# Optimization experiments

Hardware: AMD Instinct MI355X
Metric: run time of the kernel (lower is better)

## Reference

```python
import math
import jax, jax.numpy as jnp
import numpy as np

N_HEADS = 16

def setup_inputs() -> dict:
    key = jax.random.key(0)
    k1, k2, k3 = jax.random.split(key, 3)
    B, T, C = 4, 2048, 1024
    alpha = 0.5
    std = alpha * (1.0 / C) ** 0.5
    x = jax.random.normal(k1, (B, T, C), dtype=jnp.float32)
    w_attn = jax.random.normal(k2, (C, 3 * C), dtype=jnp.float32) * std
    b_attn = jnp.zeros((3 * C,), dtype=jnp.float32)
    w_proj = jax.random.normal(k3, (C, C), dtype=jnp.float32) * std
    b_proj = jnp.zeros((C,), dtype=jnp.float32)
    return {"x": x, "w_attn": w_attn, "b_attn": b_attn, "w_proj": w_proj, "b_proj": b_proj}

def reference(x, w_attn, b_attn, w_proj, b_proj):
    B, T, C = x.shape
    H = N_HEADS
    D = C // H
    qkv = x @ w_attn + b_attn                      # [B,T,3C]
    q, k, v = jnp.split(qkv, 3, axis=-1)
    # [B,T,C] -> [B,H,T,D]
    q = q.reshape(B, T, H, D).transpose(0, 2, 1, 3)
    k = k.reshape(B, T, H, D).transpose(0, 2, 1, 3)
    v = v.reshape(B, T, H, D).transpose(0, 2, 1, 3)
    att = jnp.einsum('bhqd,bhkd->bhqk', q, k) * (1.0 / math.sqrt(D))
    causal = jnp.tril(jnp.ones((T, T), dtype=bool))
    att = jnp.where(causal, att, -jnp.inf)
    att = jax.nn.softmax(att, axis=-1)
    y = jnp.einsum('bhqk,bhkd->bhqd', att, v)      # [B,H,T,D]
    y = y.transpose(0, 2, 1, 3).reshape(B, T, C)
    return y @ w_proj + b_proj
```

## Files before the change

### kernel.cpp

```cpp
#include <hip/hip_runtime.h>
#include <hip/hip_bf16.h>

typedef __bf16 bf16x8 __attribute__((ext_vector_type(8)));
typedef float f32x4 __attribute__((ext_vector_type(4)));
typedef float f32x16 __attribute__((ext_vector_type(16)));
typedef unsigned short u16x8 __attribute__((ext_vector_type(8)));
typedef unsigned short u16x4 __attribute__((ext_vector_type(4)));

#define HB 16
#define TT 2048
#define CCH 1024
#define DD 64

#define AS1 __attribute__((address_space(1)))
#define AS3 __attribute__((address_space(3)))
#define GL16(gp, lp) __builtin_amdgcn_global_load_lds((const AS1 void*)(gp), (AS3 void*)(lp), 16, 0, 0)

__device__ __forceinline__ unsigned short f2bf(float f) {
  union { __hip_bfloat16 h; unsigned short u; } cv;
  cv.h = __float2bfloat16(f);
  return cv.u;
}

__device__ __forceinline__ unsigned pack2(float lo, float hi) {
  unsigned r;
  asm("v_cvt_pk_bf16_f32 %0, %1, %2" : "=v"(r) : "v"(lo), "v"(hi));
  return r;
}

__device__ __forceinline__ f32x4 mfma16(bf16x8 a, bf16x8 b, f32x4 c) {
  return __builtin_amdgcn_mfma_f32_16x16x32_bf16(a, b, c, 0, 0, 0);
}
__device__ __forceinline__ f32x16 mfma32(bf16x8 a, bf16x8 b, f32x16 c) {
  return __builtin_amdgcn_mfma_f32_32x32x16_bf16(a, b, c, 0, 0, 0);
}

__device__ __forceinline__ f32x16 zero16() {
  f32x16 z;
  #pragma unroll
  for (int r = 0; r < 16; ++r) z[r] = 0.f;
  return z;
}


__global__ __launch_bounds__(256) void cvt_f32_bf16(const float* __restrict__ in,
                                                    unsigned short* __restrict__ out,
                                                    int n4) {
  int i = blockIdx.x * 256 + threadIdx.x;
  if (i >= n4) return;
  float4 v = reinterpret_cast<const float4*>(in)[i];
  u16x4 o;
  o.x = f2bf(v.x); o.y = f2bf(v.y); o.z = f2bf(v.z); o.w = f2bf(v.w);
  *reinterpret_cast<u16x4*>(out + (size_t)i * 4) = o;
}

__global__ __launch_bounds__(256) void transpose_cvt(const float* __restrict__ w,
                                                     unsigned short* __restrict__ wt,
                                                     int N) {
  __shared__ unsigned short t[32][33];
  int nb = blockIdx.x * 32, kb = blockIdx.y * 32;
  int tx = threadIdx.x & 31, ty = threadIdx.x >> 5;
  #pragma unroll
  for (int r = 0; r < 32; r += 8)
    t[ty + r][tx] = f2bf(w[(size_t)(kb + ty + r) * N + nb + tx]);
  __syncthreads();
  #pragma unroll
  for (int r = 0; r < 32; r += 8)
    wt[(size_t)(nb + ty + r) * 1024 + kb + tx] = t[tx][ty + r];
}


template <int EPI>
__global__ __launch_bounds__(256) void gemm_bf16(
    const unsigned short* __restrict__ A,
    const unsigned short* __restrict__ Bt,
    const float* __restrict__ bias,
    float* __restrict__ outf,
    unsigned short* __restrict__ qb,
    unsigned short* __restrict__ kb,
    unsigned short* __restrict__ vt,
    int nbx, int wpx) {
  __shared__ unsigned short As[8192];
  __shared__ unsigned short Bs[8192];
  const int bid = blockIdx.x;
  const int work = (bid & 7) * wpx + (bid >> 3);
  const int m0 = (work / nbx) * 128, n0 = (work % nbx) * 128;
  const int tid = threadIdx.x;
  const int lane = tid & 63;
  const int wid = tid >> 6;
  const int r16 = lane & 15, g = lane >> 4;
  const int wm = wid >> 1, wn = wid & 1;
  const int srow = tid >> 3;
  const int schx = (tid & 7) ^ (srow & 7);

  f32x4 acc[4][4];
  #pragma unroll
  for (int i = 0; i < 4; ++i)
    #pragma unroll
    for (int j = 0; j < 4; ++j) acc[i][j] = (f32x4){0.f, 0.f, 0.f, 0.f};

  const int rx = r16 & 7;

  for (int kt = 0; kt < 1024; kt += 64) {
    #pragma unroll
    for (int i = 0; i < 4; ++i) {
      const int row = i * 32 + srow;
      GL16(A + (size_t)(m0 + row) * 1024 + kt + schx * 8, As + i * 2048 + tid * 8);
    }
    #pragma unroll
    for (int i = 0; i < 4; ++i) {
      const int row = i * 32 + srow;
      GL16(Bt + (size_t)(n0 + row) * 1024 + kt + schx * 8, Bs + i * 2048 + tid * 8);
    }
    __syncthreads();
    #pragma unroll
    for (int h = 0; h < 2; ++h) {
      bf16x8 af[4], bfr[4];
      #pragma unroll
      for (int i = 0; i < 4; ++i)
        af[i] = *reinterpret_cast<const bf16x8*>(
            &As[(wm * 64 + i * 16 + r16) * 64 + ((g + 4 * h) ^ rx) * 8]);
      #pragma unroll
      for (int j = 0; j < 4; ++j)
        bfr[j] = *reinterpret_cast<const bf16x8*>(
            &Bs[(wn * 64 + j * 16 + r16) * 64 + ((g + 4 * h) ^ rx) * 8]);
      #pragma unroll
      for (int i = 0; i < 4; ++i)
        #pragma unroll
        for (int j = 0; j < 4; ++j)
          acc[i][j] = mfma16(af[i], bfr[j], acc[i][j]);
    }
    __syncthreads();
  }

  #pragma unroll
  for (int i = 0; i < 4; ++i) {
    #pragma unroll
    for (int j = 0; j < 4; ++j) {
      const int n = n0 + wn * 64 + j * 16 + r16;
      const int mbase = m0 + wm * 64 + i * 16 + g * 4;
      const float bi = bias[n];
      if (EPI == 1) {
        #pragma unroll
        for (int r = 0; r < 4; ++r)
          outf[(size_t)(mbase + r) * 1024 + n] = acc[i][j][r] + bi;
      } else {
        const int which = n >> 10;
        const int cc2 = n & 1023;
        const int h = cc2 >> 6, d = cc2 & 63;
        const int b = mbase >> 11, t = mbase & 2047;
        if (which == 2) {
          u16x4 o;
          #pragma unroll
          for (int r = 0; r < 4; ++r) o[r] = f2bf(acc[i][j][r] + bi);
          *reinterpret_cast<u16x4*>(
              &vt[(((size_t)b * HB + h) * DD + d) * TT + t]) = o;
        } else {
          unsigned short* dst = (which == 0) ? qb : kb;
          const float sc = (which == 0) ? 0.18033688011112042f : 1.0f;
          #pragma unroll
          for (int r = 0; r < 4; ++r)
            dst[(((size_t)b * HB + h) * TT + (t + r)) * DD + d] =
                f2bf((acc[i][j][r] + bi) * sc);
        }
      }
    }
  }
}


__global__ __launch_bounds__(256, 2) void attn_kernel(
    const unsigned short* __restrict__ qg_,
    const unsigned short* __restrict__ kg_,
    const unsigned short* __restrict__ vtg_,
    unsigned short* __restrict__ yb) {
  const int bid = blockIdx.x;
  const int work = (bid & 7) * 64 + (bid >> 3);
  const int bh = work >> 3;
  const int jb = work & 7;
  const int tid = threadIdx.x;
  const int wid = tid >> 6;
  const int lane = tid & 63;
  const int l31 = lane & 31, h = lane >> 5;
  const int lx = lane & 7;
  const unsigned short* Q = qg_ + (size_t)bh * TT * DD;
  const unsigned short* K = kg_ + (size_t)bh * TT * DD;
  const unsigned short* Vt = vtg_ + (size_t)bh * DD * TT;
  const int b = bh >> 4, hd = bh & 15;

  __shared__ unsigned short kbuf[2][4096];
  __shared__ unsigned short vbuf[2][4096];

  const int krow0 = tid >> 3;
  const int chx = (tid & 7) ^ (krow0 & 7);

#define SK(bi_, kvb_) do {                                                   \
    const unsigned short* gk_ = K + (size_t)((kvb_) + krow0) * DD + chx * 8; \
    GL16(gk_,            &kbuf[bi_][tid * 8]);                               \
    GL16(gk_ + 32 * DD,  &kbuf[bi_][2048 + tid * 8]);                        \
  } while (0)
#define SV(bi_, kvb_) do {                                                   \
    const unsigned short* gv_ = Vt + (size_t)krow0 * TT + (kvb_) + chx * 8;  \
    GL16(gv_,            &vbuf[bi_][tid * 8]);                               \
    GL16(gv_ + 32 * TT,  &vbuf[bi_][2048 + tid * 8]);                        \
  } while (0)

  #pragma unroll
  for (int part = 0; part < 2; ++part) {
    const int qg0 = (part == 0) ? jb * 128 : (15 - jb) * 128;
    const int nt = (part == 0) ? (jb + 1) * 2 : (16 - jb) * 2;
    const int qw = qg0 + wid * 32;
    const int q = qw + l31;
    const int ntw = ((qw + 31) >> 6) + 1;

    bf16x8 qf[4];
    #pragma unroll
    for (int c = 0; c < 4; ++c)
      qf[c] = *reinterpret_cast<const bf16x8*>(&Q[(size_t)q * DD + c * 16 + h * 8]);

    f32x16 y0 = zero16(), y1 = zero16();
    float lp = 0.f;

    __syncthreads();
    SK(0, 0);
    SV(0, 0);
    if (nt > 1) {
      SK(1, 64);
      SV(1, 64);
      asm volatile("s_waitcnt vmcnt(4)" ::: "memory");
    } else {
      asm volatile("s_waitcnt vmcnt(0)" ::: "memory");
    }
    __builtin_amdgcn_s_barrier();

    for (int t = 0; t < nt; ++t) {
      const unsigned short* sK = kbuf[t & 1];
      const unsigned short* sV = vbuf[t & 1];

      if (t < ntw) {
        const int kvb = t * 64;

        f32x16 z0 = zero16(), z1 = zero16();
        __builtin_amdgcn_s_setprio(1);
        #pragma unroll
        for (int c = 0; c < 4; ++c) {
          bf16x8 kf = *reinterpret_cast<const bf16x8*>(
              &sK[l31 * 64 + (((2 * c + h) ^ lx)) * 8]);
          z0 = mfma32(kf, qf[c], z0);
        }
        #pragma unroll
        for (int c = 0; c < 4; ++c) {
          bf16x8 kf = *reinterpret_cast<const bf16x8*>(
              &sK[(32 + l31) * 64 + (((2 * c + h) ^ lx)) * 8]);
          z1 = mfma32(kf, qf[c], z1);
        }
        __builtin_amdgcn_s_setprio(0);

        if (t == ntw - 1) {
          #pragma unroll
          for (int r = 0; r < 16; ++r) {
            const int kv0 = kvb + (r & 3) + 8 * (r >> 2) + 4 * h;
            if (kv0 > q) z0[r] = -1e30f;
            if (kv0 + 32 > q) z1[r] = -1e30f;
          }
        }

        float sq[8];
        #pragma unroll
        for (int i = 0; i < 4; ++i) {
          #pragma unroll
          for (int r = 0; r < 4; ++r) {
            z0[4 * i + r] = exp2f(z0[4 * i + r]);
            z1[4 * i + r] = exp2f(z1[4 * i + r]);
          }
          sq[i] = (z0[4 * i] + z0[4 * i + 1]) + (z0[4 * i + 2] + z0[4 * i + 3]);
          sq[4 + i] = (z1[4 * i] + z1[4 * i + 1]) + (z1[4 * i + 2] + z1[4 * i + 3]);
        }
        lp += ((sq[0] + sq[1]) + (sq[2] + sq[3])) +
              ((sq[4] + sq[5]) + (sq[6] + sq[7]));

        unsigned pw[16];
        #pragma unroll
        for (int w = 0; w < 8; ++w) {
          pw[w] = pack2(z0[2 * w], z0[2 * w + 1]);
          pw[8 + w] = pack2(z1[2 * w], z1[2 * w + 1]);
        }
        #pragma unroll
        for (int kb = 0; kb < 4; ++kb) {
          asm("v_permlane32_swap_b32 %0, %1"
              : "+v"(pw[4 * kb]), "+v"(pw[4 * kb + 2]));
          asm("v_permlane32_swap_b32 %0, %1"
              : "+v"(pw[4 * kb + 1]), "+v"(pw[4 * kb + 3]));
        }

        __builtin_amdgcn_s_setprio(1);
        #pragma unroll
        for (int kb = 0; kb < 4; ++kb) {
          union { unsigned w[4]; bf16x8 v; } pf;
          pf.w[0] = pw[4 * kb];
          pf.w[1] = pw[4 * kb + 1];
          pf.w[2] = pw[4 * kb + 2];
          pf.w[3] = pw[4 * kb + 3];
          bf16x8 vf0 = *reinterpret_cast<const bf16x8*>(
              &sV[l31 * 64 + (((2 * kb + h) ^ lx)) * 8]);
          y0 = mfma32(vf0, pf.v, y0);
          bf16x8 vf1 = *reinterpret_cast<const bf16x8*>(
              &sV[(32 + l31) * 64 + (((2 * kb + h) ^ lx)) * 8]);
          y1 = mfma32(vf1, pf.v, y1);
        }
        __builtin_amdgcn_s_setprio(0);
      }

      __syncthreads();
      if (t + 2 < nt) {
        SK(t & 1, (t + 2) * 64);
        SV(t & 1, (t + 2) * 64);
      }
    }

    lp += __shfl_xor(lp, 32);
    const float rl = 1.0f / lp;
    const size_t obase = ((size_t)b * TT + q) * CCH + hd * DD;
    #pragma unroll
    for (int g4 = 0; g4 < 4; ++g4) {
      const int d0 = 8 * g4 + 4 * h;
      unsigned w0 = pack2(y0[4 * g4] * rl, y0[4 * g4 + 1] * rl);
      unsigned w1 = pack2(y0[4 * g4 + 2] * rl, y0[4 * g4 + 3] * rl);
      *reinterpret_cast<uint2*>(&yb[obase + d0]) = make_uint2(w0, w1);
      unsigned w2 = pack2(y1[4 * g4] * rl, y1[4 * g4 + 1] * rl);
      unsigned w3 = pack2(y1[4 * g4 + 2] * rl, y1[4 * g4 + 3] * rl);
      *reinterpret_cast<uint2*>(&yb[obase + 32 + d0]) = make_uint2(w2, w3);
    }
  }
#undef SK
#undef SV
}


extern "C" void kernel_launch(void* const* d_in, const int* in_sizes, int n_in,
                              void* d_out, int out_size, void* d_ws, size_t ws_size,
                              hipStream_t stream) {
  const float* x      = (const float*)d_in[0];
  const float* w_attn = (const float*)d_in[1];
  const float* b_attn = (const float*)d_in[2];
  const float* w_proj = (const float*)d_in[3];
  const float* b_proj = (const float*)d_in[4];
  float* out = (float*)d_out;
  char* ws = (char*)d_ws;

  unsigned short* xb  = (unsigned short*)(ws + 0);
  unsigned short* wat = (unsigned short*)(ws + 16777216);
  unsigned short* wpt = (unsigned short*)(ws + 23068672);
  unsigned short* qb  = (unsigned short*)(ws + 25165824);
  unsigned short* kb  = (unsigned short*)(ws + 41943040);
  unsigned short* vt  = (unsigned short*)(ws + 58720256);
  unsigned short* yb  = (unsigned short*)(ws + 75497472);

  cvt_f32_bf16<<<(8192 * 1024 / 4 + 255) / 256, 256, 0, stream>>>(x, xb, 8192 * 1024 / 4);
  transpose_cvt<<<dim3(3072 / 32, 32), 256, 0, stream>>>(w_attn, wat, 3072);
  transpose_cvt<<<dim3(1024 / 32, 32), 256, 0, stream>>>(w_proj, wpt, 1024);

  gemm_bf16<0><<<1536, 256, 0, stream>>>(
      xb, wat, b_attn, nullptr, qb, kb, vt, 24, 192);

  attn_kernel<<<512, 256, 0, stream>>>(qb, kb, vt, yb);

  gemm_bf16<1><<<512, 256, 0, stream>>>(
      yb, wpt, b_proj, out, nullptr, nullptr, nullptr, 8, 64);
}
```

Measured before the change: 175.8 us.

## Drop LDS K/V staging in attention; per-wave global loads with balanced strips

Rewrites the attention kernel so each wave loads K and V tiles directly from global memory instead of cooperatively staging them into double-buffered shared memory. Work is split into 32-row query strips assigned per wave with complementary causal lengths, and the grid doubles while occupancy hint rises to 4 blocks per CU. This removes barriers and LDS traffic but gives up cross-wave reuse of K/V, increasing global/cache load traffic and exposing load latency.

```diff
diff --git a/kernel.cpp b/kernel.cpp
--- a/kernel.cpp
+++ b/kernel.cpp
@@ -169,171 +169,120 @@
 }
 
 
-__global__ __launch_bounds__(256, 2) void attn_kernel(
+__global__ __launch_bounds__(256, 4) void attn_kernel(
     const unsigned short* __restrict__ qg_,
     const unsigned short* __restrict__ kg_,
     const unsigned short* __restrict__ vtg_,
     unsigned short* __restrict__ yb) {
   const int bid = blockIdx.x;
-  const int work = (bid & 7) * 64 + (bid >> 3);
-  const int bh = work >> 3;
-  const int jb = work & 7;
-  const int tid = threadIdx.x;
-  const int wid = tid >> 6;
-  const int lane = tid & 63;
+  const int work = (bid & 7) * 128 + (bid >> 3);
+  const int bh = work >> 4;
+  const int jb = work & 15;
+  const int wid = threadIdx.x >> 6;
+  const int lane = threadIdx.x & 63;
   const int l31 = lane & 31, h = lane >> 5;
-  const int lx = lane & 7;
-  const unsigned short* Q = qg_ + (size_t)bh * TT * DD;
-  const unsigned short* K = kg_ + (size_t)bh * TT * DD;
-  const unsigned short* Vt = vtg_ + (size_t)bh * DD * TT;
+  const int s = (wid == 0) ? jb : (wid == 1) ? (31 - jb)
+              : (wid == 2) ? (32 + jb) : (63 - jb);
+  const unsigned short* __restrict__ Q = qg_ + (size_t)bh * TT * DD;
+  const unsigned short* __restrict__ K = kg_ + (size_t)bh * TT * DD;
+  const unsigned short* __restrict__ Vt = vtg_ + (size_t)bh * DD * TT;
   const int b = bh >> 4, hd = bh & 15;
 
-  __shared__ unsigned short kbuf[2][4096];
-  __shared__ unsigned short vbuf[2][4096];
-
-  const int krow0 = tid >> 3;
-  const int chx = (tid & 7) ^ (krow0 & 7);
-
-#define SK(bi_, kvb_) do {                                                   \
-    const unsigned short* gk_ = K + (size_t)((kvb_) + krow0) * DD + chx * 8; \
-    GL16(gk_,            &kbuf[bi_][tid * 8]);                               \
-    GL16(gk_ + 32 * DD,  &kbuf[bi_][2048 + tid * 8]);                        \
-  } while (0)
-#define SV(bi_, kvb_) do {                                                   \
-    const unsigned short* gv_ = Vt + (size_t)krow0 * TT + (kvb_) + chx * 8;  \
-    GL16(gv_,            &vbuf[bi_][tid * 8]);                               \
-    GL16(gv_ + 32 * TT,  &vbuf[bi_][2048 + tid * 8]);                        \
-  } while (0)
-
-  #pragma unroll
-  for (int part = 0; part < 2; ++part) {
-    const int qg0 = (part == 0) ? jb * 128 : (15 - jb) * 128;
-    const int nt = (part == 0) ? (jb + 1) * 2 : (16 - jb) * 2;
-    const int qw = qg0 + wid * 32;
-    const int q = qw + l31;
-    const int ntw = ((qw + 31) >> 6) + 1;
-
-    bf16x8 qf[4];
-    #pragma unroll
-    for (int c = 0; c < 4; ++c)
-      qf[c] = *reinterpret_cast<const bf16x8*>(&Q[(size_t)q * DD + c * 16 + h * 8]);
-
-    f32x16 y0 = zero16(), y1 = zero16();
-    float lp = 0.f;
-
-    __syncthreads();
-    SK(0, 0);
-    SV(0, 0);
-    if (nt > 1) {
-      SK(1, 64);
-      SV(1, 64);
-      asm volatile("s_waitcnt vmcnt(4)" ::: "memory");
-    } else {
-      asm volatile("s_waitcnt vmcnt(0)" ::: "memory");
-    }
-    __builtin_amdgcn_s_barrier();
-
-    for (int t = 0; t < nt; ++t) {
-      const unsigned short* sK = kbuf[t & 1];
-      const unsigned short* sV = vbuf[t & 1];
-
-      if (t < ntw) {
-        const int kvb = t * 64;
-
-        f32x16 z0 = zero16(), z1 = zero16();
-        __builtin_amdgcn_s_setprio(1);
-        #pragma unroll
-        for (int c = 0; c < 4; ++c) {
-          bf16x8 kf = *reinterpret_cast<const bf16x8*>(
-              &sK[l31 * 64 + (((2 * c + h) ^ lx)) * 8]);
-          z0 = mfma32(kf, qf[c], z0);
-        }
-        #pragma unroll
-        for (int c = 0; c < 4; ++c) {
-          bf16x8 kf = *reinterpret_cast<const bf16x8*>(
-              &sK[(32 + l31) * 64 + (((2 * c + h) ^ lx)) * 8]);
-          z1 = mfma32(kf, qf[c], z1);
-        }
-        __builtin_amdgcn_s_setprio(0);
-
-        if (t == ntw - 1) {
-          #pragma unroll
-          for (int r = 0; r < 16; ++r) {
-            const int kv0 = kvb + (r & 3) + 8 * (r >> 2) + 4 * h;
-            if (kv0 > q) z0[r] = -1e30f;
-            if (kv0 + 32 > q) z1[r] = -1e30f;
-          }
-        }
-
-        float sq[8];
-        #pragma unroll
-        for (int i = 0; i < 4; ++i) {
-          #pragma unroll
-          for (int r = 0; r < 4; ++r) {
-            z0[4 * i + r] = exp2f(z0[4 * i + r]);
-            z1[4 * i + r] = exp2f(z1[4 * i + r]);
-          }
-          sq[i] = (z0[4 * i] + z0[4 * i + 1]) + (z0[4 * i + 2] + z0[4 * i + 3]);
-          sq[4 + i] = (z1[4 * i] + z1[4 * i + 1]) + (z1[4 * i + 2] + z1[4 * i + 3]);
-        }
-        lp += ((sq[0] + sq[1]) + (sq[2] + sq[3])) +
-              ((sq[4] + sq[5]) + (sq[6] + sq[7]));
-
-        unsigned pw[16];
-        #pragma unroll
-        for (int w = 0; w < 8; ++w) {
-          pw[w] = pack2(z0[2 * w], z0[2 * w + 1]);
-          pw[8 + w] = pack2(z1[2 * w], z1[2 * w + 1]);
-        }
-        #pragma unroll
-        for (int kb = 0; kb < 4; ++kb) {
-          asm("v_permlane32_swap_b32 %0, %1"
-              : "+v"(pw[4 * kb]), "+v"(pw[4 * kb + 2]));
-          asm("v_permlane32_swap_b32 %0, %1"
-              : "+v"(pw[4 * kb + 1]), "+v"(pw[4 * kb + 3]));
-        }
-
-        __builtin_amdgcn_s_setprio(1);
-        #pragma unroll
-        for (int kb = 0; kb < 4; ++kb) {
-          union { unsigned w[4]; bf16x8 v; } pf;
-          pf.w[0] = pw[4 * kb];
-          pf.w[1] = pw[4 * kb + 1];
-          pf.w[2] = pw[4 * kb + 2];
-          pf.w[3] = pw[4 * kb + 3];
-          bf16x8 vf0 = *reinterpret_cast<const bf16x8*>(
-              &sV[l31 * 64 + (((2 * kb + h) ^ lx)) * 8]);
-          y0 = mfma32(vf0, pf.v, y0);
-          bf16x8 vf1 = *reinterpret_cast<const bf16x8*>(
-              &sV[(32 + l31) * 64 + (((2 * kb + h) ^ lx)) * 8]);
-          y1 = mfma32(vf1, pf.v, y1);
-        }
-        __builtin_amdgcn_s_setprio(0);
+  const int q = 32 * s + l31;
+  const int nt = (s >> 1) + 1;
+
+  bf16x8 qf[4];
+  #pragma unroll
+  for (int c = 0; c < 4; ++c)
+    qf[c] = *reinterpret_cast<const bf16x8*>(&Q[(size_t)q * DD + c * 16 + h * 8]);
+
+  const unsigned short* __restrict__ K0 = K + (size_t)l31 * DD + h * 8;
+  const unsigned short* __restrict__ K1 = K + (size_t)(32 + l31) * DD + h * 8;
+  const unsigned short* __restrict__ V0 = Vt + (size_t)l31 * TT + h * 8;
+  const unsigned short* __restrict__ V1 = Vt + (size_t)(32 + l31) * TT + h * 8;
+
+  f32x16 y0 = zero16(), y1 = zero16();
+  float lp = 0.f;
+
+  for (int t = 0; t < nt; ++t) {
+    const int kvb = t * 64;
+
+    f32x16 z0 = zero16(), z1 = zero16();
+    #pragma unroll
+    for (int c = 0; c < 4; ++c) {
+      bf16x8 kf = *reinterpret_cast<const bf16x8*>(&K0[(size_t)kvb * DD + c * 16]);
+      z0 = mfma32(kf, qf[c], z0);
+    }
+    #pragma unroll
+    for (int c = 0; c < 4; ++c) {
+      bf16x8 kf = *reinterpret_cast<const bf16x8*>(&K1[(size_t)kvb * DD + c * 16]);
+      z1 = mfma32(kf, qf[c], z1);
+    }
+
+    if (t == nt - 1) {
+      #pragma unroll
+      for (int r = 0; r < 16; ++r) {
+        const int kv0 = kvb + (r & 3) + 8 * (r >> 2) + 4 * h;
+        if (kv0 > q) z0[r] = -1e30f;
+        if (kv0 + 32 > q) z1[r] = -1e30f;
       }
-
-      __syncthreads();
-      if (t + 2 < nt) {
-        SK(t & 1, (t + 2) * 64);
-        SV(t & 1, (t + 2) * 64);
+    }
+
+    float sq[8];
+    #pragma unroll
+    for (int i = 0; i < 4; ++i) {
+      #pragma unroll
+      for (int r = 0; r < 4; ++r) {
+        z0[4 * i + r] = exp2f(z0[4 * i + r]);
+        z1[4 * i + r] = exp2f(z1[4 * i + r]);
       }
-    }
-
-    lp += __shfl_xor(lp, 32);
-    const float rl = 1.0f / lp;
-    const size_t obase = ((size_t)b * TT + q) * CCH + hd * DD;
-    #pragma unroll
-    for (int g4 = 0; g4 < 4; ++g4) {
-      const int d0 = 8 * g4 + 4 * h;
-      unsigned w0 = pack2(y0[4 * g4] * rl, y0[4 * g4 + 1] * rl);
-      unsigned w1 = pack2(y0[4 * g4 + 2] * rl, y0[4 * g4 + 3] * rl);
-      *reinterpret_cast<uint2*>(&yb[obase + d0]) = make_uint2(w0, w1);
-      unsigned w2 = pack2(y1[4 * g4] * rl, y1[4 * g4 + 1] * rl);
-      unsigned w3 = pack2(y1[4 * g4 + 2] * rl, y1[4 * g4 + 3] * rl);
-      *reinterpret_cast<uint2*>(&yb[obase + 32 + d0]) = make_uint2(w2, w3);
+      sq[i] = (z0[4 * i] + z0[4 * i + 1]) + (z0[4 * i + 2] + z0[4 * i + 3]);
+      sq[4 + i] = (z1[4 * i] + z1[4 * i + 1]) + (z1[4 * i + 2] + z1[4 * i + 3]);
+    }
+    lp += ((sq[0] + sq[1]) + (sq[2] + sq[3])) +
+          ((sq[4] + sq[5]) + (sq[6] + sq[7]));
+
+    unsigned pw[16];
+    #pragma unroll
+    for (int w = 0; w < 8; ++w) {
+      pw[w] = pack2(z0[2 * w], z0[2 * w + 1]);
+      pw[8 + w] = pack2(z1[2 * w], z1[2 * w + 1]);
+    }
+    #pragma unroll
+    for (int kb = 0; kb < 4; ++kb) {
+      asm("v_permlane32_swap_b32 %0, %1"
+          : "+v"(pw[4 * kb]), "+v"(pw[4 * kb + 2]));
+      asm("v_permlane32_swap_b32 %0, %1"
+          : "+v"(pw[4 * kb + 1]), "+v"(pw[4 * kb + 3]));
+    }
+
+    #pragma unroll
+    for (int kb = 0; kb < 4; ++kb) {
+      union { unsigned w[4]; bf16x8 v; } pf;
+      pf.w[0] = pw[4 * kb];
+      pf.w[1] = pw[4 * kb + 1];
+      pf.w[2] = pw[4 * kb + 2];
+      pf.w[3] = pw[4 * kb + 3];
+      bf16x8 vf0 = *reinterpret_cast<const bf16x8*>(&V0[kvb + kb * 16]);
+      y0 = mfma32(vf0, pf.v, y0);
+      bf16x8 vf1 = *reinterpret_cast<const bf16x8*>(&V1[kvb + kb * 16]);
+      y1 = mfma32(vf1, pf.v, y1);
     }
   }
-#undef SK
-#undef SV
+
+  lp += __shfl_xor(lp, 32);
+  const float rl = 1.0f / lp;
+  const size_t obase = ((size_t)b * TT + q) * CCH + hd * DD;
+  #pragma unroll
+  for (int g4 = 0; g4 < 4; ++g4) {
+    const int d0 = 8 * g4 + 4 * h;
+    unsigned w0 = pack2(y0[4 * g4] * rl, y0[4 * g4 + 1] * rl);
+    unsigned w1 = pack2(y0[4 * g4 + 2] * rl, y0[4 * g4 + 3] * rl);
+    *reinterpret_cast<uint2*>(&yb[obase + d0]) = make_uint2(w0, w1);
+    unsigned w2 = pack2(y1[4 * g4] * rl, y1[4 * g4 + 1] * rl);
+    unsigned w3 = pack2(y1[4 * g4 + 2] * rl, y1[4 * g4 + 3] * rl);
+    *reinterpret_cast<uint2*>(&yb[obase + 32 + d0]) = make_uint2(w2, w3);
+  }
 }
 
 
@@ -363,7 +312,7 @@
   gemm_bf16<0><<<1536, 256, 0, stream>>>(
       xb, wat, b_attn, nullptr, qb, kb, vt, 24, 192);
 
-  attn_kernel<<<512, 256, 0, stream>>>(qb, kb, vt, yb);
+  attn_kernel<<<1024, 256, 0, stream>>>(qb, kb, vt, yb);
 
   gemm_bf16<1><<<512, 256, 0, stream>>>(
       yb, wpt, b_proj, out, nullptr, nullptr, nullptr, 8, 64);
```

Result: slower. 252.6 us (+43.7%).
